# Optimization experiments

Measured on AMD Instinct MI355X. Metric: run time of the kernel, lower is better.

## Reference

```python
import jax, jax.numpy as jnp
import numpy as np

EPS = 1e-8  # torch F.cosine_similarity default eps
NEG = -1e9  # masked_fill value


def setup_inputs() -> dict:
    key = jax.random.key(0)
    k1, k2, k3 = jax.random.split(key, 3)
    B, Sq, Sk, D = 4, 2048, 2048, 1024
    query = jax.random.normal(k1, (B, Sq, 1, D), dtype=jnp.float32)
    key_t = jax.random.normal(k2, (B, 1, Sk, D), dtype=jnp.float32)
    mask = jax.random.randint(k3, (B, Sk), 0, 2, dtype=jnp.int32)
    return {"query": query, "key": key_t, "mask": mask}


def reference(query, key, mask):
    # query: [B, Sq, 1, D], key: [B, 1, Sk, D]
    q = query[:, :, 0, :]  # [B, Sq, D]
    k = key[:, 0, :, :]    # [B, Sk, D]
    # cosine_similarity(q, k, dim=3) = (q.k) / (max(|q|,eps) * max(|k|,eps))
    qn = jnp.maximum(jnp.linalg.norm(q, axis=-1), EPS)  # [B, Sq]
    kn = jnp.maximum(jnp.linalg.norm(k, axis=-1), EPS)  # [B, Sk]
    dot = jnp.einsum('bqd,bkd->bqk', q, k)              # [B, Sq, Sk]
    scores = dot / (qn[:, :, None] * kn[:, None, :])
    # mask.unsqueeze(1).repeat(1, Sq, 1) -> broadcast [B, 1, Sk] over Sq
    scores = jnp.where(mask[:, None, :] == 0, NEG, scores)
    return scores
```

## Files before the change

### kernel.cpp

```cpp
#include <hip/hip_runtime.h>
#include <hip/hip_bf16.h>
#include <stdint.h>


constexpr int B_  = 4;
constexpr int SQ  = 2048;
constexpr int SK  = 2048;
constexpr int D_  = 1024;
constexpr int BM  = 128;
constexpr int BN  = 128;
constexpr int BK  = 64;

typedef __attribute__((ext_vector_type(8)))  short    short8;
typedef __attribute__((ext_vector_type(4)))  float    f32x4;
typedef __attribute__((ext_vector_type(16))) float    f32x16;
typedef __attribute__((ext_vector_type(4)))  unsigned uint4v;
typedef unsigned int u32;

__device__ inline unsigned pack_bf16(float lo, float hi) {
  union { float f; unsigned u; } a, b;
  a.f = lo; b.f = hi;
  return __builtin_amdgcn_perm(b.u, a.u, 0x07060302u);
}

__device__ inline void async_ld16(const void* g, void* l) {
  __builtin_amdgcn_global_load_lds((const __attribute__((address_space(1))) u32*)g,
                                   (__attribute__((address_space(3))) u32*)l, 16, 0, 0);
}

constexpr int ROWS_Q = B_ * SQ;
constexpr int ROWS_T = B_ * (SQ + SK);

__global__ __launch_bounds__(256) void convert_norm(
    const float* __restrict__ Q, const float* __restrict__ Km,
    unsigned short* __restrict__ Qb, unsigned short* __restrict__ Kb,
    float* __restrict__ invQ, float* __restrict__ invK)
{
  const int row  = blockIdx.x * 4 + (threadIdx.x >> 6);
  const int lane = threadIdx.x & 63;

  const float* src; unsigned short* dst; float* inv;
  if (row < ROWS_Q) {
    src = Q  + (size_t)row * D_;
    dst = Qb + (size_t)row * D_;
    inv = invQ + row;
  } else {
    int r = row - ROWS_Q;
    src = Km + (size_t)r * D_;
    dst = Kb + (size_t)r * D_;
    inv = invK + r;
  }

  const f32x4* s4 = (const f32x4*)(src + lane * 16);
  f32x4 v[4];
  #pragma unroll
  for (int i = 0; i < 4; ++i) v[i] = s4[i];

  float ss = 0.0f;
  unsigned p[8];
  #pragma unroll
  for (int i = 0; i < 4; ++i) {
    p[2*i]   = pack_bf16(v[i].x, v[i].y);
    p[2*i+1] = pack_bf16(v[i].z, v[i].w);
    ss += v[i].x*v[i].x + v[i].y*v[i].y + v[i].z*v[i].z + v[i].w*v[i].w;
  }
  uint4v w0 = {p[0], p[1], p[2], p[3]};
  uint4v w1 = {p[4], p[5], p[6], p[7]};
  uint4v* d4 = (uint4v*)(dst + lane * 16);
  d4[0] = w0; d4[1] = w1;

  #pragma unroll
  for (int off = 32; off > 0; off >>= 1) ss += __shfl_xor(ss, off);
  if (lane == 0) *inv = 1.0f / fmaxf(sqrtf(ss), 1e-8f);
}

__global__ __launch_bounds__(256, 4) void ca_gemm_bf(
    const unsigned short* __restrict__ Qb,
    const unsigned short* __restrict__ Kb,
    const float* __restrict__ invQ,
    const float* __restrict__ invK,
    const int*   __restrict__ mask,
    float*       __restrict__ out)
{
  __shared__ __align__(16) unsigned short As[BM * BK];
  __shared__ __align__(16) unsigned short Bs[BN * BK];

  const int tid  = threadIdx.x;
  const int lane = tid & 63;
  const int w    = tid >> 6;

  const int lid = blockIdx.x;
  const int xcd = lid & 7;
  const int idx = lid >> 3;
  const int sq  = xcd * 2 + (idx >> 6);
  const int b   = sq >> 2;
  const int qd  = sq & 3;
  const int ty  = (qd >> 1) * 8 + ((idx >> 3) & 7);
  const int tx  = (qd & 1) * 8 + (idx & 7);
  const int tm0 = ty * BM;
  const int tn0 = tx * BN;

  const int srow   = lane >> 3;
  const int gchunk = (lane & 7) ^ srow;

  const char* qrow = (const char*)(Qb + ((size_t)b * SQ + tm0 + w * 32 + srow) * D_) + gchunk * 16;
  const char* krow = (const char*)(Kb + ((size_t)b * SK + tn0 + w * 32 + srow) * D_) + gchunk * 16;
  const size_t rstep8 = (size_t)8 * D_ * 2;

  unsigned short* ldsA = &As[(size_t)(w * 32) * BK];
  unsigned short* ldsB = &Bs[(size_t)(w * 32) * BK];

  f32x16 acc[2][2];
  #pragma unroll
  for (int i = 0; i < 2; ++i)
    #pragma unroll
    for (int j = 0; j < 2; ++j)
      #pragma unroll
      for (int r = 0; r < 16; ++r) acc[i][j][r] = 0.0f;

  const int wm = (w >> 1) * 64;
  const int wn = (w & 1) * 64;
  const int ln = lane & 31;
  const int h  = lane >> 5;

  for (int k0 = 0; k0 < D_; k0 += BK) {
    __syncthreads();
    const size_t kb = (size_t)k0 * 2;
    #pragma unroll
    for (int i = 0; i < 4; ++i)
      async_ld16(qrow + kb + i * rstep8, ldsA + i * 8 * BK);
    #pragma unroll
    for (int i = 0; i < 4; ++i)
      async_ld16(krow + kb + i * rstep8, ldsB + i * 8 * BK);
    __syncthreads();

    #pragma unroll
    for (int s = 0; s < 4; ++s) {
      const int c = 2 * s + h;
      const int ra0 = wm + ln, ra1 = wm + 32 + ln;
      const int rb0 = wn + ln, rb1 = wn + 32 + ln;
      short8 a0 = *(const short8*)&As[(size_t)ra0 * BK + (size_t)((c ^ (ra0 & 7)) * 8)];
      short8 a1 = *(const short8*)&As[(size_t)ra1 * BK + (size_t)((c ^ (ra1 & 7)) * 8)];
      short8 b0 = *(const short8*)&Bs[(size_t)rb0 * BK + (size_t)((c ^ (rb0 & 7)) * 8)];
      short8 b1 = *(const short8*)&Bs[(size_t)rb1 * BK + (size_t)((c ^ (rb1 & 7)) * 8)];
      acc[0][0] = __builtin_amdgcn_mfma_f32_32x32x16_bf16(a0, b0, acc[0][0], 0, 0, 0);
      acc[0][1] = __builtin_amdgcn_mfma_f32_32x32x16_bf16(a0, b1, acc[0][1], 0, 0, 0);
      acc[1][0] = __builtin_amdgcn_mfma_f32_32x32x16_bf16(a1, b0, acc[1][0], 0, 0, 0);
      acc[1][1] = __builtin_amdgcn_mfma_f32_32x32x16_bf16(a1, b1, acc[1][1], 0, 0, 0);
    }
  }

  #pragma unroll
  for (int tj = 0; tj < 2; ++tj) {
    const int gc = tn0 + wn + tj * 32 + ln;
    const int mk = mask[b * SK + gc];
    const float ibv = invK[b * SK + gc];
    #pragma unroll
    for (int ti = 0; ti < 2; ++ti) {
      #pragma unroll
      for (int reg = 0; reg < 16; ++reg) {
        const int row = wm + ti * 32 + (reg & 3) + 8 * (reg >> 2) + 4 * h;
        const float iav = invQ[b * SQ + tm0 + row];
        float v = mk ? acc[ti][tj][reg] * iav * ibv : -1000000000.0f;
        out[((size_t)b * SQ + tm0 + row) * SK + gc] = v;
      }
    }
  }
}

constexpr int LDK = 40;

__global__ __launch_bounds__(256, 2) void ca_gemm(
    const float* __restrict__ Q, const float* __restrict__ Km,
    const int* __restrict__ mask, float* __restrict__ out)
{
  __shared__ __align__(16) short As[BM * LDK];
  __shared__ __align__(16) short Bs[BN * LDK];
  __shared__ float ssA_part[256];
  __shared__ float ssB_part[256];
  __shared__ float invA[BM];
  __shared__ float invB[BN];

  const int tid  = threadIdx.x;
  const int lane = tid & 63;
  const int w    = tid >> 6;
  const int b    = blockIdx.z;
  const int tm0  = blockIdx.y * BM;
  const int tn0  = blockIdx.x * BN;

  const int ra = tid >> 1;
  const int ka = (tid & 1) * 16;

  const float* qp = Q  + ((size_t)b * SQ + tm0 + ra) * D_ + ka;
  const float* kp = Km + ((size_t)b * SK + tn0 + ra) * D_ + ka;

  f32x4 zero4 = {0.0f, 0.0f, 0.0f, 0.0f};
  f32x4 acc[4][4];
  #pragma unroll
  for (int i = 0; i < 4; ++i)
    #pragma unroll
    for (int j = 0; j < 4; ++j) acc[i][j] = zero4;

  float ssA = 0.0f, ssB = 0.0f;

  const int wm = (w >> 1) * 64;
  const int wn = (w & 1) * 64;
  const int lr = lane & 15;
  const int lq = lane >> 4;

  short* aw = &As[ra * LDK + ka];
  short* bw = &Bs[ra * LDK + ka];

  for (int k0 = 0; k0 < D_; k0 += 32) {
    f32x4 av[4], bv[4];
    #pragma unroll
    for (int i = 0; i < 4; ++i) av[i] = *(const f32x4*)(qp + 4 * i);
    #pragma unroll
    for (int i = 0; i < 4; ++i) bv[i] = *(const f32x4*)(kp + 4 * i);
    qp += 32; kp += 32;

    unsigned pa[8], pb[8];
    #pragma unroll
    for (int i = 0; i < 4; ++i) {
      pa[2*i]   = pack_bf16(av[i].x, av[i].y);
      pa[2*i+1] = pack_bf16(av[i].z, av[i].w);
      pb[2*i]   = pack_bf16(bv[i].x, bv[i].y);
      pb[2*i+1] = pack_bf16(bv[i].z, bv[i].w);
      ssA += av[i].x*av[i].x + av[i].y*av[i].y + av[i].z*av[i].z + av[i].w*av[i].w;
      ssB += bv[i].x*bv[i].x + bv[i].y*bv[i].y + bv[i].z*bv[i].z + bv[i].w*bv[i].w;
    }

    __syncthreads();
    {
      uint4v wa0 = {pa[0], pa[1], pa[2], pa[3]};
      uint4v wa1 = {pa[4], pa[5], pa[6], pa[7]};
      uint4v wb0 = {pb[0], pb[1], pb[2], pb[3]};
      uint4v wb1 = {pb[4], pb[5], pb[6], pb[7]};
      *(uint4v*)(aw)     = wa0;
      *(uint4v*)(aw + 8) = wa1;
      *(uint4v*)(bw)     = wb0;
      *(uint4v*)(bw + 8) = wb1;
    }
    __syncthreads();

    short8 af[4], bf[4];
    #pragma unroll
    for (int t = 0; t < 4; ++t)
      af[t] = *(const short8*)&As[(wm + t * 16 + lr) * LDK + lq * 8];
    #pragma unroll
    for (int t = 0; t < 4; ++t)
      bf[t] = *(const short8*)&Bs[(wn + t * 16 + lr) * LDK + lq * 8];

    #pragma unroll
    for (int i = 0; i < 4; ++i)
      #pragma unroll
      for (int j = 0; j < 4; ++j)
        acc[i][j] = __builtin_amdgcn_mfma_f32_16x16x32_bf16(af[i], bf[j], acc[i][j], 0, 0, 0);
  }

  ssA_part[tid] = ssA;
  ssB_part[tid] = ssB;
  __syncthreads();
  if (tid < BM) {
    float s = ssA_part[2 * tid] + ssA_part[2 * tid + 1];
    invA[tid] = 1.0f / fmaxf(sqrtf(s), 1e-8f);
  } else {
    int r = tid - BM;
    float s = ssB_part[2 * r] + ssB_part[2 * r + 1];
    invB[r] = 1.0f / fmaxf(sqrtf(s), 1e-8f);
  }
  __syncthreads();

  #pragma unroll
  for (int tn = 0; tn < 4; ++tn) {
    const int lc = wn + tn * 16 + lr;
    const int gc = tn0 + lc;
    const int mk = mask[b * SK + gc];
    const float ibv = invB[lc];
    #pragma unroll
    for (int tm = 0; tm < 4; ++tm) {
      const int lrow = wm + tm * 16 + lq * 4;
      #pragma unroll
      for (int r = 0; r < 4; ++r) {
        float v = mk ? acc[tm][tn][r] * invA[lrow + r] * ibv : -1000000000.0f;
        out[((size_t)b * SQ + tm0 + lrow + r) * SK + gc] = v;
      }
    }
  }
}

extern "C" void kernel_launch(void* const* d_in, const int* in_sizes, int n_in,
                              void* d_out, int out_size, void* d_ws, size_t ws_size,
                              hipStream_t stream) {
  const float* Q    = (const float*)d_in[0];
  const float* Km   = (const float*)d_in[1];
  const int*   mask = (const int*)d_in[2];
  float*       out  = (float*)d_out;

  const size_t nQ   = (size_t)B_ * SQ * D_;
  const size_t nK   = (size_t)B_ * SK * D_;
  const size_t need = (nQ + nK) * 2 + (size_t)B_ * (SQ + SK) * 4;
  if (ws_size >= need) {
    unsigned short* Qb = (unsigned short*)d_ws;
    unsigned short* Kb = Qb + nQ;
    float*          iQ = (float*)(Kb + nK);
    float*          iK = iQ + (size_t)B_ * SQ;
    convert_norm<<<ROWS_T / 4, 256, 0, stream>>>(Q, Km, Qb, Kb, iQ, iK);
    ca_gemm_bf<<<dim3(1024), dim3(256), 0, stream>>>(Qb, Kb, iQ, iK, mask, out);
  } else {
    dim3 grid(SK / BN, SQ / BM, B_);
    ca_gemm<<<grid, dim3(256), 0, stream>>>(Q, Km, mask, out);
  }
}
```

Before: 158.4 us.

## Fuse bf16 conversion and norm pass into GEMM kernel with per-panel flag sync

Merges the separate convert/normalize kernel into the GEMM kernel. Each of the 1024 blocks first converts 16 rows of Q or K to bf16 and computes their inverse norms, then bumps a per-panel atomic counter. Before its GEMM tile, a block spins until the A and B panels it needs are ready, and falls back to redoing the conversion itself on timeout. This removes one kernel launch and the gap between kernels, but adds a memset, spin-wait latency and a dependency on all blocks being co-resident.

```diff
diff --git a/kernel.cpp b/kernel.cpp
--- a/kernel.cpp
+++ b/kernel.cpp
@@ -11,6 +11,11 @@
 constexpr int BN  = 128;
 constexpr int BK  = 64;
 
+constexpr int ROWS_Q = B_ * SQ;
+constexpr int ROWS_T = B_ * (SQ + SK);
+constexpr int NPANEL = ROWS_T / 128;
+constexpr int SPIN_MAX = 1 << 18;
+
 typedef __attribute__((ext_vector_type(8)))  short    short8;
 typedef __attribute__((ext_vector_type(4)))  float    f32x4;
 typedef __attribute__((ext_vector_type(16))) float    f32x16;
@@ -28,24 +33,19 @@
                                    (__attribute__((address_space(3))) u32*)l, 16, 0, 0);
 }
 
-constexpr int ROWS_Q = B_ * SQ;
-constexpr int ROWS_T = B_ * (SQ + SK);
-
-__global__ __launch_bounds__(256) void convert_norm(
+__device__ __attribute__((noinline)) void conv_row(
+    int grow, int lane,
     const float* __restrict__ Q, const float* __restrict__ Km,
     unsigned short* __restrict__ Qb, unsigned short* __restrict__ Kb,
     float* __restrict__ invQ, float* __restrict__ invK)
 {
-  const int row  = blockIdx.x * 4 + (threadIdx.x >> 6);
-  const int lane = threadIdx.x & 63;
-
   const float* src; unsigned short* dst; float* inv;
-  if (row < ROWS_Q) {
-    src = Q  + (size_t)row * D_;
-    dst = Qb + (size_t)row * D_;
-    inv = invQ + row;
+  if (grow < ROWS_Q) {
+    src = Q  + (size_t)grow * D_;
+    dst = Qb + (size_t)grow * D_;
+    inv = invQ + grow;
   } else {
-    int r = row - ROWS_Q;
+    int r = grow - ROWS_Q;
     src = Km + (size_t)r * D_;
     dst = Kb + (size_t)r * D_;
     inv = invK + r;
@@ -74,22 +74,34 @@
   if (lane == 0) *inv = 1.0f / fmaxf(sqrtf(ss), 1e-8f);
 }
 
-__global__ __launch_bounds__(256, 4) void ca_gemm_bf(
-    const unsigned short* __restrict__ Qb,
-    const unsigned short* __restrict__ Kb,
-    const float* __restrict__ invQ,
-    const float* __restrict__ invK,
+__global__ __launch_bounds__(256, 4) void ca_coop(
+    const float* __restrict__ Q,
+    const float* __restrict__ Km,
     const int*   __restrict__ mask,
-    float*       __restrict__ out)
+    float*       __restrict__ out,
+    unsigned short* __restrict__ Qb,
+    unsigned short* __restrict__ Kb,
+    float* __restrict__ invQ,
+    float* __restrict__ invK,
+    int*   __restrict__ flags)
 {
   __shared__ __align__(16) unsigned short As[BM * BK];
   __shared__ __align__(16) unsigned short Bs[BN * BK];
+  __shared__ int timeout;
 
   const int tid  = threadIdx.x;
   const int lane = tid & 63;
   const int w    = tid >> 6;
-
-  const int lid = blockIdx.x;
+  const int lid  = blockIdx.x;
+
+  #pragma unroll
+  for (int j = 0; j < 4; ++j)
+    conv_row(lid * 16 + j * 4 + w, lane, Q, Km, Qb, Kb, invQ, invK);
+  __threadfence();
+  __syncthreads();
+  if (tid == 0)
+    __hip_atomic_fetch_add(&flags[lid >> 3], 1, __ATOMIC_ACQ_REL, __HIP_MEMORY_SCOPE_AGENT);
+
   const int xcd = lid & 7;
   const int idx = lid >> 3;
   const int sq  = xcd * 2 + (idx >> 6);
@@ -99,6 +111,27 @@
   const int tx  = (qd & 1) * 8 + (idx & 7);
   const int tm0 = ty * BM;
   const int tn0 = tx * BN;
+  const int pA  = b * 16 + ty;
+  const int pB  = 64 + b * 16 + tx;
+
+  if (tid == 0) {
+    timeout = 0;
+    int spins = 0;
+    while ((__hip_atomic_load(&flags[pA], __ATOMIC_ACQUIRE, __HIP_MEMORY_SCOPE_AGENT) < 8 ||
+            __hip_atomic_load(&flags[pB], __ATOMIC_ACQUIRE, __HIP_MEMORY_SCOPE_AGENT) < 8)) {
+      if (++spins >= SPIN_MAX) { timeout = 1; break; }
+    }
+  }
+  __syncthreads();
+  if (timeout) {
+    for (int i = 0; i < 32; ++i)
+      conv_row(pA * 128 + i * 4 + w, lane, Q, Km, Qb, Kb, invQ, invK);
+    for (int i = 0; i < 32; ++i)
+      conv_row(ROWS_Q + (pB - 64) * 128 + i * 4 + w, lane, Q, Km, Qb, Kb, invQ, invK);
+    __threadfence();
+    __syncthreads();
+  }
+  __threadfence();
 
   const int srow   = lane >> 3;
   const int gchunk = (lane & 7) ^ srow;
@@ -299,14 +332,18 @@
 
   const size_t nQ   = (size_t)B_ * SQ * D_;
   const size_t nK   = (size_t)B_ * SK * D_;
-  const size_t need = (nQ + nK) * 2 + (size_t)B_ * (SQ + SK) * 4;
+  const size_t nInv = (size_t)B_ * (SQ + SK);
+  const size_t need = (nQ + nK) * 2 + nInv * 4 + NPANEL * 4;
   if (ws_size >= need) {
     unsigned short* Qb = (unsigned short*)d_ws;
     unsigned short* Kb = Qb + nQ;
     float*          iQ = (float*)(Kb + nK);
     float*          iK = iQ + (size_t)B_ * SQ;
-    convert_norm<<<ROWS_T / 4, 256, 0, stream>>>(Q, Km, Qb, Kb, iQ, iK);
-    ca_gemm_bf<<<dim3(1024), dim3(256), 0, stream>>>(Qb, Kb, iQ, iK, mask, out);
+    int*         flags = (int*)(iK + (size_t)B_ * SK);
+
+    hipMemsetAsync(flags, 0, NPANEL * 4, stream);
+    ca_coop<<<dim3(1024), dim3(256), 0, stream>>>(Q, Km, mask, out,
+                                                  Qb, Kb, iQ, iK, flags);
   } else {
     dim3 grid(SK / BN, SQ / BM, B_);
     ca_gemm<<<grid, dim3(256), 0, stream>>>(Q, Km, mask, out);
```

New measurement: 418.9 us. 2.65x slower.
